# Optimization experiments

Hardware: AMD Instinct MI355X
Metric: run time of the kernel (lower is better)

The kernel has to match this reference:

```python
import jax, jax.numpy as jnp
import numpy as np

N_NODES = 100000
N_EDGES = 600000
HID = 128
N_ETYPES = 8


def setup_inputs() -> dict:
    key = jax.random.key(0)
    ks = jax.random.split(key, 10)
    s = 1.0 / np.sqrt(HID)
    return {
        "h": jax.random.normal(ks[0], (N_NODES, HID), dtype=jnp.float32),
        "edge_index": jax.random.randint(ks[1], (2, N_EDGES), 0, N_NODES, dtype=jnp.int64),
        "edge_type": jax.random.randint(ks[2], (N_EDGES,), 0, N_ETYPES, dtype=jnp.int64),
        # per-edge-type Linear(hidden, hidden): weight (T, H_out, H_in) stored as (T, H_in, H_out) for einsum
        "message_W": jax.random.uniform(ks[3], (N_ETYPES, HID, HID), jnp.float32, -s, s),
        "message_b": jax.random.uniform(ks[4], (N_ETYPES, HID), jnp.float32, -s, s),
        # GRUCell params (torch layout): w_ih (3H, H), w_hh (3H, H), b_ih (3H,), b_hh (3H,)
        "gru_w_ih": jax.random.uniform(ks[5], (3 * HID, HID), jnp.float32, -s, s),
        "gru_w_hh": jax.random.uniform(ks[6], (3 * HID, HID), jnp.float32, -s, s),
        "gru_b_ih": jax.random.uniform(ks[7], (3 * HID,), jnp.float32, -s, s),
        "gru_b_hh": jax.random.uniform(ks[8], (3 * HID,), jnp.float32, -s, s),
    }


def reference(h, edge_index, edge_type, message_W, message_b,
              gru_w_ih, gru_w_hh, gru_b_ih, gru_b_hh):
    num_nodes = h.shape[0]
    src, dst = edge_index[0], edge_index[1]

    # Transform every node by every edge-type Linear once: (N, T, H).
    # Equivalent to per-type msg = h[src] @ W[t].T + b[t] gathered by edge type.
    all_msgs = jnp.einsum('nh,thd->ntd', h, message_W) + message_b  # (N, T, H)
    msg = all_msgs[src, edge_type]                                   # (E, H) gather
    messages = jax.ops.segment_sum(msg, dst, num_segments=num_nodes)  # scatter-add

    # GRUCell: r,z,n gates (torch semantics)
    gi = messages @ gru_w_ih.T + gru_b_ih  # (N, 3H)
    gh = h @ gru_w_hh.T + gru_b_hh         # (N, 3H)
    i_r, i_z, i_n = jnp.split(gi, 3, axis=-1)
    h_r, h_z, h_n = jnp.split(gh, 3, axis=-1)
    r = jax.nn.sigmoid(i_r + h_r)
    z = jax.nn.sigmoid(i_z + h_z)
    n = jnp.tanh(i_n + r * h_n)
    return (1.0 - z) * n + z * h
```

## Files before the change

kernel.cpp:

```cpp
#include <hip/hip_runtime.h>

#define HID 128
#define NTY 8

typedef __attribute__((ext_vector_type(8))) short bf16x8;
typedef __attribute__((ext_vector_type(4))) float f32x4;

__device__ __forceinline__ unsigned short f2bf(float x) {
    unsigned u = __float_as_uint(x);
    u += 0x7FFF + ((u >> 16) & 1);
    return (unsigned short)(u >> 16);
}
__device__ __forceinline__ float bf2f(unsigned short s) {
    return __uint_as_float(((unsigned)s) << 16);
}
__device__ __forceinline__ float sigmoidf_fast(float x) {
    return 1.f / (1.f + __expf(-x));
}
__device__ __forceinline__ float tanhf_fast(float x) {
    return 1.f - 2.f / (1.f + __expf(2.f * x));
}

__global__ void conv_all_kernel(const float* __restrict__ h, unsigned short* __restrict__ hbf, int nh,
                                const float* __restrict__ W, unsigned short* __restrict__ wfr,
                                const float* __restrict__ wih, const float* __restrict__ whh,
                                unsigned short* __restrict__ wpkf,
                                int* __restrict__ sortedT, int capE,
                                int* __restrict__ deg, int N, int* __restrict__ tcnt)
{
    int i = blockIdx.x * 256 + threadIdx.x;
    if (i < nh) { hbf[i] = f2bf(h[i]); return; }
    i -= nh;
    if (i < 131072) {
        int e = i & 7, lane = (i >> 3) & 63, cb = (i >> 9) & 7, kc = (i >> 12) & 3, t = i >> 14;
        int lr = lane & 15, quad = lane >> 4;
        int d = cb * 16 + lr;
        int k = kc * 32 + quad * 8 + e;
        wfr[i] = f2bf(W[(t << 14) + (k << 7) + d]);
        return;
    }
    i -= 131072;
    if (i < 98304) {
        int e = i & 7, lane = (i >> 3) & 63, f = i >> 9;
        int ct = f & 7, fg = f >> 3;
        int g3 = fg % 3, kc = fg / 3;
        int lr = lane & 15, quad = lane >> 4;
        int d = ct * 16 + lr;
        int kk = quad * 8 + e;
        float v;
        if (kc < 4) v = wih[(g3 * 128 + d) * 128 + kc * 32 + kk];
        else        v = whh[(g3 * 128 + d) * 128 + (kc - 4) * 32 + kk];
        wpkf[i] = f2bf(v);
        return;
    }
    i -= 98304;
    if (i < capE) { sortedT[i] = -1; return; }
    i -= capE;
    if (i < N) { deg[i] = 0; return; }
    i -= N;
    if (i < NTY) tcnt[i] = 0;
}

__global__ void hist_kernel(const int* __restrict__ etype, const int* __restrict__ ei,
                            int E, int* __restrict__ tcnt, int* __restrict__ deg) {
    __shared__ int lc[NTY];
    if (threadIdx.x < NTY) lc[threadIdx.x] = 0;
    __syncthreads();
    int stride = gridDim.x * blockDim.x;
    for (int i = blockIdx.x * blockDim.x + threadIdx.x; i < E; i += stride) {
        atomicAdd(&lc[etype[i]], 1);
        if (deg) atomicAdd(&deg[ei[E + i]], 1);
    }
    __syncthreads();
    if (threadIdx.x < NTY) atomicAdd(&tcnt[threadIdx.x], lc[threadIdx.x]);
}

__global__ void scanA_kernel(const int* __restrict__ deg, int* __restrict__ start,
                             int* __restrict__ bsum, int N) {
    __shared__ int s[256];
    int i = blockIdx.x * 256 + threadIdx.x;
    int v = (i < N) ? deg[i] : 0;
    s[threadIdx.x] = v;
    __syncthreads();
    for (int off = 1; off < 256; off <<= 1) {
        int t = (threadIdx.x >= off) ? s[threadIdx.x - off] : 0;
        __syncthreads();
        s[threadIdx.x] += t;
        __syncthreads();
    }
    if (i < N) start[i] = s[threadIdx.x] - v;
    if (threadIdx.x == 255) bsum[blockIdx.x] = s[255];
}

__global__ void scanB_kernel(int* __restrict__ bsum, int nb,
                             const int* __restrict__ tcnt, int* __restrict__ tcur) {
    __shared__ int s[512];
    int tx = threadIdx.x;
    int v = (tx < nb) ? bsum[tx] : 0;
    s[tx] = v;
    __syncthreads();
    for (int off = 1; off < 512; off <<= 1) {
        int t = (tx >= off) ? s[tx - off] : 0;
        __syncthreads();
        s[tx] += t;
        __syncthreads();
    }
    if (tx < nb) bsum[tx] = s[tx] - v;
    if (tx == 0) {
        int off = 0;
        for (int t = 0; t < NTY; ++t) { tcur[t] = off; off += (tcnt[t] + 127) & ~127; }
    }
}

__global__ void scanC_kernel(int* __restrict__ start, const int* __restrict__ bsum,
                             int* __restrict__ dcur, int N, int E) {
    int i = blockIdx.x * 256 + threadIdx.x;
    if (i < N) {
        int v = start[i] + bsum[blockIdx.x];
        start[i] = v;
        dcur[i] = v;
    }
    if (i == 0) start[N] = E;
}

__global__ __launch_bounds__(256) void scatter_agg(
    const int* __restrict__ etype, const int* __restrict__ ei, int E,
    int* __restrict__ tcur, int* __restrict__ dcur,
    int* __restrict__ sortedT, int* __restrict__ q, int mode)
{
    __shared__ int lcnt[NTY];
    __shared__ int lbase[NTY];
    int tx = threadIdx.x;
    int chunk = (E + gridDim.x - 1) / gridDim.x;
    int s = blockIdx.x * chunk;
    int e = s + chunk; if (e > E) e = E;
    if (tx < NTY) lcnt[tx] = 0;
    __syncthreads();
    for (int i = s + tx; i < e; i += 256)
        atomicAdd(&lcnt[etype[i]], 1);
    __syncthreads();
    if (tx < NTY) {
        lbase[tx] = atomicAdd(&tcur[tx], lcnt[tx]);
        lcnt[tx] = 0;
    }
    __syncthreads();
    for (int i = s + tx; i < e; i += 256) {
        int t = etype[i];
        int lp = atomicAdd(&lcnt[t], 1);
        sortedT[lbase[t] + lp] = i;
        if (mode) q[i] = atomicAdd(&dcur[ei[E + i]], 1);
    }
}

__global__ __launch_bounds__(256) void msg_gemm(
    const unsigned short* __restrict__ hbf, const int* __restrict__ ei, int E,
    const int* __restrict__ etype, const unsigned short* __restrict__ wfr,
    const float* __restrict__ bias, const int* __restrict__ sortedT,
    const int* __restrict__ q, unsigned short* __restrict__ M,
    float* __restrict__ msum, int mode)
{
    __shared__ unsigned short hs[128][136];
    __shared__ int srcs[128], aux[128];
    __shared__ int stype;

    int tx = threadIdx.x;
    int base = blockIdx.x * 128;
    if (tx < 128) {
        int id = sortedT[base + tx];
        srcs[tx] = (id >= 0) ? ei[id] : -1;
        aux[tx]  = (id >= 0) ? (mode ? ei[E + id] : q[id]) : -1;
    }
    if (tx == 0) { int id0 = sortedT[base]; stype = (id0 >= 0) ? etype[id0] : -1; }
    __syncthreads();
    int t = stype;
    if (t < 0) return;

    for (int f = tx; f < 2048; f += 256) {
        int row = f >> 4, c8 = (f & 15) * 8;
        int s = srcs[row]; if (s < 0) s = 0;
        *(uint4*)&hs[row][c8] = *(const uint4*)&hbf[(size_t)s * 128 + c8];
    }
    __syncthreads();

    int lane = tx & 63, w = tx >> 6;
    int r0 = (w >> 1) * 64, c0 = (w & 1) * 64;
    int lr = lane & 15, quad = lane >> 4;
    f32x4 acc[4][4] = {};

    const unsigned short* wt = wfr + (t << 14) + ((unsigned)(c0 >> 4) << 9) + (lane << 3);
    #pragma unroll
    for (int kc = 0; kc < 4; ++kc) {
        bf16x8 af[4], wf[4];
        #pragma unroll
        for (int rb = 0; rb < 4; ++rb) af[rb] = *(const bf16x8*)&hs[r0 + rb * 16 + lr][kc * 32 + quad * 8];
        #pragma unroll
        for (int cb = 0; cb < 4; ++cb) wf[cb] = *(const bf16x8*)&wt[(kc << 12) + (cb << 9)];
        #pragma unroll
        for (int rb = 0; rb < 4; ++rb)
            #pragma unroll
            for (int cb = 0; cb < 4; ++cb)
                acc[rb][cb] = __builtin_amdgcn_mfma_f32_16x16x32_bf16(wf[cb], af[rb], acc[rb][cb], 0, 0, 0);
    }

    float4 bv4[4];
    #pragma unroll
    for (int cb = 0; cb < 4; ++cb)
        bv4[cb] = *(const float4*)&bias[t * 128 + c0 + cb * 16 + quad * 4];

    #pragma unroll
    for (int rb = 0; rb < 4; ++rb) {
        int e = r0 + rb * 16 + lr;
        int mr = aux[e];
        if (mr < 0) continue;
        #pragma unroll
        for (int cb = 0; cb < 4; ++cb) {
            int d0 = c0 + cb * 16 + quad * 4;
            f32x4 a = acc[rb][cb];
            if (mode) {
                atomicAdd(&msum[(size_t)mr * 128 + d0 + 0], a[0] + bv4[cb].x);
                atomicAdd(&msum[(size_t)mr * 128 + d0 + 1], a[1] + bv4[cb].y);
                atomicAdd(&msum[(size_t)mr * 128 + d0 + 2], a[2] + bv4[cb].z);
                atomicAdd(&msum[(size_t)mr * 128 + d0 + 3], a[3] + bv4[cb].w);
            } else {
                uint2 v;
                v.x = (unsigned)f2bf(a[0] + bv4[cb].x) | ((unsigned)f2bf(a[1] + bv4[cb].y) << 16);
                v.y = (unsigned)f2bf(a[2] + bv4[cb].z) | ((unsigned)f2bf(a[3] + bv4[cb].w) << 16);
                *(uint2*)&M[(size_t)mr * 128 + d0] = v;
            }
        }
    }
}

__global__ __launch_bounds__(256) void gru_fused(
    const unsigned short* __restrict__ M, const int* __restrict__ start,
    const float* __restrict__ msum_fb, const unsigned short* __restrict__ hbf,
    const unsigned short* __restrict__ wpkf, const float* __restrict__ bih,
    const float* __restrict__ bhh, const float* __restrict__ hf,
    float* __restrict__ out, int N, int mode)
{
    __shared__ unsigned short As[4][2048];

    int tx = threadIdx.x;
    int n0 = blockIdx.x * 64;

    {
        int node = tx >> 2, qd = tx & 3;
        int n = n0 + node;
        int nc = (n < N) ? n : N - 1;
        float a[32];
        #pragma unroll
        for (int j = 0; j < 32; ++j) a[j] = 0.f;
        if (mode == 0) {
            int s = start[nc], e = start[nc + 1];
            uint4 c0v, c1v, c2v, c3v;
            if (s < e) {
                const unsigned short* Mp = M + (size_t)s * 128 + qd * 32;
                c0v = *(const uint4*)(Mp);
                c1v = *(const uint4*)(Mp + 8);
                c2v = *(const uint4*)(Mp + 16);
                c3v = *(const uint4*)(Mp + 24);
            }
            for (int r = s; r < e; ++r) {
                uint4 p0 = c0v, p1 = c1v, p2 = c2v, p3 = c3v;
                if (r + 1 < e) {
                    const unsigned short* Mn = M + (size_t)(r + 1) * 128 + qd * 32;
                    c0v = *(const uint4*)(Mn);
                    c1v = *(const uint4*)(Mn + 8);
                    c2v = *(const uint4*)(Mn + 16);
                    c3v = *(const uint4*)(Mn + 24);
                }
                const unsigned short* q0 = (const unsigned short*)&p0;
                const unsigned short* q1 = (const unsigned short*)&p1;
                const unsigned short* q2 = (const unsigned short*)&p2;
                const unsigned short* q3 = (const unsigned short*)&p3;
                #pragma unroll
                for (int u = 0; u < 8; ++u) {
                    a[u]      += bf2f(q0[u]);
                    a[8 + u]  += bf2f(q1[u]);
                    a[16 + u] += bf2f(q2[u]);
                    a[24 + u] += bf2f(q3[u]);
                }
            }
        } else {
            #pragma unroll
            for (int j = 0; j < 8; ++j) {
                float4 v = *(const float4*)&msum_fb[(size_t)nc * 128 + qd * 32 + j * 4];
                a[j * 4 + 0] = v.x; a[j * 4 + 1] = v.y; a[j * 4 + 2] = v.z; a[j * 4 + 3] = v.w;
            }
        }
        unsigned short tmp[32];
        #pragma unroll
        for (int j = 0; j < 32; ++j) tmp[j] = f2bf(a[j]);
        int lrw = node & 15, wv = node >> 4;
        #pragma unroll
        for (int j = 0; j < 4; ++j) {
            int byte = (lrw << 8) + (qd << 6) + (j << 4);
            byte ^= (lrw & 7) << 4;
            *(uint4*)((char*)&As[wv][0] + byte) = *(const uint4*)&tmp[j * 8];
        }
    }
    __syncthreads();

    int lane = tx & 63, w = tx >> 6;
    int lr = lane & 15, quad = lane >> 4;
    int node = n0 + w * 16 + lr;
    bool valid = node < N;
    int nc = valid ? node : (N - 1);
    unsigned short* AsW = &As[w][0];

    bf16x8 afh[4];
    {
        const unsigned short* hrow = hbf + ((size_t)nc << 7) + (quad << 3);
        #pragma unroll
        for (int k4 = 0; k4 < 4; ++k4) afh[k4] = *(const bf16x8*)&hrow[k4 * 32];
    }
    const unsigned short* wg = wpkf + (lane << 3);

    #pragma unroll
    for (int dh = 0; dh < 2; ++dh) {
        f32x4 aR[4] = {}, aZ[4] = {}, aH[4] = {};
        #pragma unroll
        for (int kc = 0; kc < 8; ++kc) {
            bf16x8 af;
            if (kc < 4) {
                int byte = ((lr << 8) + (kc << 6) + (quad << 4)) ^ ((lr & 7) << 4);
                af = *(const bf16x8*)((char*)AsW + byte);
            } else {
                af = afh[kc - 4];
            }
            #pragma unroll
            for (int c = 0; c < 4; ++c) {
                int ct = dh * 4 + c;
                bf16x8 wfR = *(const bf16x8*)&wg[(unsigned)((kc * 3 + 0) * 8 + ct) << 9];
                aR[c] = __builtin_amdgcn_mfma_f32_16x16x32_bf16(wfR, af, aR[c], 0, 0, 0);
                bf16x8 wfZ = *(const bf16x8*)&wg[(unsigned)((kc * 3 + 1) * 8 + ct) << 9];
                aZ[c] = __builtin_amdgcn_mfma_f32_16x16x32_bf16(wfZ, af, aZ[c], 0, 0, 0);
                if (kc >= 4) {
                    bf16x8 wfH = *(const bf16x8*)&wg[(unsigned)((kc * 3 + 2) * 8 + ct) << 9];
                    aH[c] = __builtin_amdgcn_mfma_f32_16x16x32_bf16(wfH, af, aH[c], 0, 0, 0);
                }
            }
        }
        f32x4 rv[4], zv[4];
        #pragma unroll
        for (int c = 0; c < 4; ++c) {
            int d0 = (dh * 4 + c) * 16 + quad * 4;
            f32x4 bir = *(const f32x4*)&bih[d0],       bhr = *(const f32x4*)&bhh[d0];
            f32x4 biz = *(const f32x4*)&bih[128 + d0], bhz = *(const f32x4*)&bhh[128 + d0];
            f32x4 bin = *(const f32x4*)&bih[256 + d0], bhn = *(const f32x4*)&bhh[256 + d0];
            #pragma unroll
            for (int j = 0; j < 4; ++j) {
                rv[c][j] = sigmoidf_fast(aR[c][j] + bir[j] + bhr[j]);
                zv[c][j] = sigmoidf_fast(aZ[c][j] + biz[j] + bhz[j]);
                aH[c][j] = bin[j] + rv[c][j] * (aH[c][j] + bhn[j]);
            }
        }
        #pragma unroll
        for (int kc = 0; kc < 4; ++kc) {
            int byte = ((lr << 8) + (kc << 6) + (quad << 4)) ^ ((lr & 7) << 4);
            bf16x8 af = *(const bf16x8*)((char*)AsW + byte);
            #pragma unroll
            for (int c = 0; c < 4; ++c) {
                bf16x8 wfH = *(const bf16x8*)&wg[(unsigned)((kc * 3 + 2) * 8 + dh * 4 + c) << 9];
                aH[c] = __builtin_amdgcn_mfma_f32_16x16x32_bf16(wfH, af, aH[c], 0, 0, 0);
            }
        }
        if (valid) {
            #pragma unroll
            for (int c = 0; c < 4; ++c) {
                int d0 = (dh * 4 + c) * 16 + quad * 4;
                f32x4 h0 = *(const f32x4*)&hf[(size_t)node * 128 + d0];
                f32x4 o;
                #pragma unroll
                for (int j = 0; j < 4; ++j) {
                    float nn = tanhf_fast(aH[c][j]);
                    o[j] = (1.f - zv[c][j]) * nn + zv[c][j] * h0[j];
                }
                *(f32x4*)&out[(size_t)node * 128 + d0] = o;
            }
        }
    }
}

extern "C" void kernel_launch(void* const* d_in, const int* in_sizes, int n_in,
                              void* d_out, int out_size, void* d_ws, size_t ws_size,
                              hipStream_t stream)
{
    const float* h     = (const float*)d_in[0];
    const int*   ei    = (const int*)d_in[1];
    const int*   etype = (const int*)d_in[2];
    const float* W     = (const float*)d_in[3];
    const float* b     = (const float*)d_in[4];
    const float* wih   = (const float*)d_in[5];
    const float* whh   = (const float*)d_in[6];
    const float* bih   = (const float*)d_in[7];
    const float* bhh   = (const float*)d_in[8];
    float* out = (float*)d_out;

    int E = in_sizes[1] / 2;
    int N = in_sizes[0] / HID;
    int capE = ((E + 127) / 128 + NTY) * 128;
    int nbA = (N + 255) / 256;

    char* p = (char*)d_ws;
    auto alloc = [&](size_t bytes) { char* r = p; p += (bytes + 255) & ~(size_t)255; return r; };
    unsigned short* hbf  = (unsigned short*)alloc((size_t)N * 128 * 2);
    unsigned short* wfr  = (unsigned short*)alloc((size_t)131072 * 2);
    unsigned short* wpkf = (unsigned short*)alloc((size_t)98304 * 2);
    int* tcnt    = (int*)alloc(NTY * 4);
    int* tcur    = (int*)alloc(NTY * 4);
    int* sortedT = (int*)alloc((size_t)capE * 4);
    unsigned short* M = (unsigned short*)alloc((size_t)E * 128 * 2);
    int* q     = (int*)alloc((size_t)E * 4);
    int* deg   = (int*)alloc((size_t)N * 4);
    int* start = (int*)alloc((size_t)(N + 1) * 4);
    int* dcur  = (int*)alloc((size_t)N * 4);
    int* bsum  = (int*)alloc(512 * 4);
    int mode = ((size_t)(p - (char*)d_ws) <= ws_size) ? 0 : 1;

    if (mode == 1) hipMemsetAsync(out, 0, (size_t)N * 128 * 4, stream);

    int totalConv = N * 128 + 131072 + 98304 + capE + N + NTY;
    conv_all_kernel<<<(totalConv + 255) / 256, 256, 0, stream>>>(
        h, hbf, N * 128, W, wfr, wih, whh, wpkf, sortedT, capE, deg, N, tcnt);

    hist_kernel<<<1024, 256, 0, stream>>>(etype, ei, E, tcnt, (mode == 0) ? deg : nullptr);
    if (mode == 0)
        scanA_kernel<<<nbA, 256, 0, stream>>>(deg, start, bsum, N);
    scanB_kernel<<<1, 512, 0, stream>>>(bsum, nbA, tcnt, tcur);
    if (mode == 0)
        scanC_kernel<<<nbA, 256, 0, stream>>>(start, bsum, dcur, N, E);
    scatter_agg<<<256, 256, 0, stream>>>(etype, ei, E, tcur, dcur, sortedT, q, (mode == 0) ? 1 : 0);

    msg_gemm<<<capE / 128, 256, 0, stream>>>(hbf, ei, E, etype, wfr, b, sortedT, q, M, out, mode);
    gru_fused<<<(N + 63) / 64, 256, 0, stream>>>(M, start, out, hbf, wpkf, bih, bhh, h, out, N, mode);
}
```

Measured before the change: 404.5 us.

## Balance CSR segment reduction across wave lanes with LDS float atomics

Replaces the per-node serial walk over CSR message rows, where four threads each handled a node and the loop length followed that node's degree, with a wave-level sweep. Each wave streams all rows of its 16 nodes in a contiguous range, four rows at a time, and accumulates into an fp32 LDS tile with shared-memory atomics. The GEMM A operand is then converted from fp32 LDS to bf16 with a packed convert instruction. This balances load across lanes when degrees vary, at the cost of many LDS atomics and a larger fp32 LDS footprint that may lower occupancy.

```diff
diff --git a/kernel.cpp b/kernel.cpp
--- a/kernel.cpp
+++ b/kernel.cpp
@@ -19,6 +19,11 @@
 }
 __device__ __forceinline__ float tanhf_fast(float x) {
     return 1.f - 2.f / (1.f + __expf(2.f * x));
+}
+__device__ __forceinline__ unsigned cvt_pk_bf16(float lo, float hi) {
+    unsigned r;
+    asm("v_cvt_pk_bf16_f32 %0, %1, %2" : "=v"(r) : "v"(lo), "v"(hi));
+    return r;
 }
 
 __global__ void conv_all_kernel(const float* __restrict__ h, unsigned short* __restrict__ hbf, int nh,
@@ -238,75 +243,55 @@
     const float* __restrict__ bhh, const float* __restrict__ hf,
     float* __restrict__ out, int N, int mode)
 {
-    __shared__ unsigned short As[4][2048];
+    __shared__ __align__(16) float macc[64][132];
+    __shared__ int bnds_l[65];
 
     int tx = threadIdx.x;
     int n0 = blockIdx.x * 64;
-
-    {
-        int node = tx >> 2, qd = tx & 3;
-        int n = n0 + node;
-        int nc = (n < N) ? n : N - 1;
-        float a[32];
-        #pragma unroll
-        for (int j = 0; j < 32; ++j) a[j] = 0.f;
-        if (mode == 0) {
-            int s = start[nc], e = start[nc + 1];
-            uint4 c0v, c1v, c2v, c3v;
-            if (s < e) {
-                const unsigned short* Mp = M + (size_t)s * 128 + qd * 32;
-                c0v = *(const uint4*)(Mp);
-                c1v = *(const uint4*)(Mp + 8);
-                c2v = *(const uint4*)(Mp + 16);
-                c3v = *(const uint4*)(Mp + 24);
-            }
-            for (int r = s; r < e; ++r) {
-                uint4 p0 = c0v, p1 = c1v, p2 = c2v, p3 = c3v;
-                if (r + 1 < e) {
-                    const unsigned short* Mn = M + (size_t)(r + 1) * 128 + qd * 32;
-                    c0v = *(const uint4*)(Mn);
-                    c1v = *(const uint4*)(Mn + 8);
-                    c2v = *(const uint4*)(Mn + 16);
-                    c3v = *(const uint4*)(Mn + 24);
-                }
-                const unsigned short* q0 = (const unsigned short*)&p0;
-                const unsigned short* q1 = (const unsigned short*)&p1;
-                const unsigned short* q2 = (const unsigned short*)&p2;
-                const unsigned short* q3 = (const unsigned short*)&p3;
-                #pragma unroll
-                for (int u = 0; u < 8; ++u) {
-                    a[u]      += bf2f(q0[u]);
-                    a[8 + u]  += bf2f(q1[u]);
-                    a[16 + u] += bf2f(q2[u]);
-                    a[24 + u] += bf2f(q3[u]);
-                }
-            }
-        } else {
-            #pragma unroll
-            for (int j = 0; j < 8; ++j) {
-                float4 v = *(const float4*)&msum_fb[(size_t)nc * 128 + qd * 32 + j * 4];
-                a[j * 4 + 0] = v.x; a[j * 4 + 1] = v.y; a[j * 4 + 2] = v.z; a[j * 4 + 3] = v.w;
-            }
-        }
-        unsigned short tmp[32];
-        #pragma unroll
-        for (int j = 0; j < 32; ++j) tmp[j] = f2bf(a[j]);
-        int lrw = node & 15, wv = node >> 4;
-        #pragma unroll
-        for (int j = 0; j < 4; ++j) {
-            int byte = (lrw << 8) + (qd << 6) + (j << 4);
-            byte ^= (lrw & 7) << 4;
-            *(uint4*)((char*)&As[wv][0] + byte) = *(const uint4*)&tmp[j * 8];
-        }
-    }
-    __syncthreads();
-
     int lane = tx & 63, w = tx >> 6;
     int lr = lane & 15, quad = lane >> 4;
+
+    for (int i = tx; i < 64 * 132 / 4; i += 256)
+        ((f32x4*)macc)[i] = f32x4{0.f, 0.f, 0.f, 0.f};
+    if (mode == 0 && tx <= 64) {
+        int idx = n0 + tx; if (idx > N) idx = N;
+        bnds_l[tx] = start[idx];
+    }
+    __syncthreads();
+
+    if (mode == 0) {
+        int row_off = quad;
+        int c = lr;
+        int lo = bnds_l[w * 16], hi = bnds_l[w * 16 + 16];
+        int cur = w * 16;
+        int nxt = bnds_l[cur + 1];
+        int r = lo + row_off;
+        uint4 v = {};
+        if (r < hi) v = *(const uint4*)&M[(size_t)r * 128 + c * 8];
+        while (r < hi) {
+            int rn = r + 4;
+            uint4 vn = {};
+            if (rn < hi) vn = *(const uint4*)&M[(size_t)rn * 128 + c * 8];
+            while (r >= nxt) { ++cur; nxt = bnds_l[cur + 1]; }
+            const unsigned short* pv = (const unsigned short*)&v;
+            float* mrow = &macc[cur][c * 8];
+            #pragma unroll
+            for (int j = 0; j < 8; ++j) atomicAdd(&mrow[j], bf2f(pv[j]));
+            v = vn; r = rn;
+        }
+    } else {
+        for (int i = tx; i < 2048; i += 256) {
+            int node = i >> 5, q4 = (i & 31) * 4;
+            int n = n0 + node; int nc2 = (n < N) ? n : N - 1;
+            *(f32x4*)&macc[node][q4] = *(const f32x4*)&msum_fb[(size_t)nc2 * 128 + q4];
+        }
+    }
+    __syncthreads();
+
     int node = n0 + w * 16 + lr;
+    int mrow_i = w * 16 + lr;
     bool valid = node < N;
     int nc = valid ? node : (N - 1);
-    unsigned short* AsW = &As[w][0];
 
     bf16x8 afh[4];
     {
@@ -323,58 +308,70 @@
         for (int kc = 0; kc < 8; ++kc) {
             bf16x8 af;
             if (kc < 4) {
-                int byte = ((lr << 8) + (kc << 6) + (quad << 4)) ^ ((lr & 7) << 4);
-                af = *(const bf16x8*)((char*)AsW + byte);
+                const float* mp = &macc[mrow_i][kc * 32 + quad * 8];
+                f32x4 L = *(const f32x4*)mp, H = *(const f32x4*)(mp + 4);
+                int4 au;
+                au.x = (int)cvt_pk_bf16(L[0], L[1]);
+                au.y = (int)cvt_pk_bf16(L[2], L[3]);
+                au.z = (int)cvt_pk_bf16(H[0], H[1]);
+                au.w = (int)cvt_pk_bf16(H[2], H[3]);
+                af = *(const bf16x8*)&au;
             } else {
                 af = afh[kc - 4];
             }
             #pragma unroll
-            for (int c = 0; c < 4; ++c) {
-                int ct = dh * 4 + c;
+            for (int cg = 0; cg < 4; ++cg) {
+                int ct = dh * 4 + cg;
                 bf16x8 wfR = *(const bf16x8*)&wg[(unsigned)((kc * 3 + 0) * 8 + ct) << 9];
-                aR[c] = __builtin_amdgcn_mfma_f32_16x16x32_bf16(wfR, af, aR[c], 0, 0, 0);
+                aR[cg] = __builtin_amdgcn_mfma_f32_16x16x32_bf16(wfR, af, aR[cg], 0, 0, 0);
                 bf16x8 wfZ = *(const bf16x8*)&wg[(unsigned)((kc * 3 + 1) * 8 + ct) << 9];
-                aZ[c] = __builtin_amdgcn_mfma_f32_16x16x32_bf16(wfZ, af, aZ[c], 0, 0, 0);
+                aZ[cg] = __builtin_amdgcn_mfma_f32_16x16x32_bf16(wfZ, af, aZ[cg], 0, 0, 0);
                 if (kc >= 4) {
                     bf16x8 wfH = *(const bf16x8*)&wg[(unsigned)((kc * 3 + 2) * 8 + ct) << 9];
-                    aH[c] = __builtin_amdgcn_mfma_f32_16x16x32_bf16(wfH, af, aH[c], 0, 0, 0);
+                    aH[cg] = __builtin_amdgcn_mfma_f32_16x16x32_bf16(wfH, af, aH[cg], 0, 0, 0);
                 }
             }
         }
         f32x4 rv[4], zv[4];
         #pragma unroll
-        for (int c = 0; c < 4; ++c) {
-            int d0 = (dh * 4 + c) * 16 + quad * 4;
+        for (int cg = 0; cg < 4; ++cg) {
+            int d0 = (dh * 4 + cg) * 16 + quad * 4;
             f32x4 bir = *(const f32x4*)&bih[d0],       bhr = *(const f32x4*)&bhh[d0];
             f32x4 biz = *(const f32x4*)&bih[128 + d0], bhz = *(const f32x4*)&bhh[128 + d0];
             f32x4 bin = *(const f32x4*)&bih[256 + d0], bhn = *(const f32x4*)&bhh[256 + d0];
             #pragma unroll
             for (int j = 0; j < 4; ++j) {
-                rv[c][j] = sigmoidf_fast(aR[c][j] + bir[j] + bhr[j]);
-                zv[c][j] = sigmoidf_fast(aZ[c][j] + biz[j] + bhz[j]);
-                aH[c][j] = bin[j] + rv[c][j] * (aH[c][j] + bhn[j]);
+                rv[cg][j] = sigmoidf_fast(aR[cg][j] + bir[j] + bhr[j]);
+                zv[cg][j] = sigmoidf_fast(aZ[cg][j] + biz[j] + bhz[j]);
+                aH[cg][j] = bin[j] + rv[cg][j] * (aH[cg][j] + bhn[j]);
             }
         }
         #pragma unroll
         for (int kc = 0; kc < 4; ++kc) {
-            int byte = ((lr << 8) + (kc << 6) + (quad << 4)) ^ ((lr & 7) << 4);
-            bf16x8 af = *(const bf16x8*)((char*)AsW + byte);
-            #pragma unroll
-            for (int c = 0; c < 4; ++c) {
-                bf16x8 wfH = *(const bf16x8*)&wg[(unsigned)((kc * 3 + 2) * 8 + dh * 4 + c) << 9];
-                aH[c] = __builtin_amdgcn_mfma_f32_16x16x32_bf16(wfH, af, aH[c], 0, 0, 0);
+            const float* mp = &macc[mrow_i][kc * 32 + quad * 8];
+            f32x4 L = *(const f32x4*)mp, H = *(const f32x4*)(mp + 4);
+            int4 au;
+            au.x = (int)cvt_pk_bf16(L[0], L[1]);
+            au.y = (int)cvt_pk_bf16(L[2], L[3]);
+            au.z = (int)cvt_pk_bf16(H[0], H[1]);
+            au.w = (int)cvt_pk_bf16(H[2], H[3]);
+            bf16x8 af = *(const bf16x8*)&au;
+            #pragma unroll
+            for (int cg = 0; cg < 4; ++cg) {
+                bf16x8 wfH = *(const bf16x8*)&wg[(unsigned)((kc * 3 + 2) * 8 + dh * 4 + cg) << 9];
+                aH[cg] = __builtin_amdgcn_mfma_f32_16x16x32_bf16(wfH, af, aH[cg], 0, 0, 0);
             }
         }
         if (valid) {
             #pragma unroll
-            for (int c = 0; c < 4; ++c) {
-                int d0 = (dh * 4 + c) * 16 + quad * 4;
+            for (int cg = 0; cg < 4; ++cg) {
+                int d0 = (dh * 4 + cg) * 16 + quad * 4;
                 f32x4 h0 = *(const f32x4*)&hf[(size_t)node * 128 + d0];
                 f32x4 o;
                 #pragma unroll
                 for (int j = 0; j < 4; ++j) {
-                    float nn = tanhf_fast(aH[c][j]);
-                    o[j] = (1.f - zv[c][j]) * nn + zv[c][j] * h0[j];
+                    float nn = tanhf_fast(aH[cg][j]);
+                    o[j] = (1.f - zv[cg][j]) * nn + zv[cg][j] * h0[j];
                 }
                 *(f32x4*)&out[(size_t)node * 128 + d0] = o;
             }
```

After: 735.8 us. 81.9% more time.

## Stage dst-sorted message rows cooperatively in LDS before per-node reduction

Applied to the files above, without the earlier changes.

Instead of each node's four threads walking their own CSR segment of the message buffer with per-thread software prefetch, the block now loads its contiguous 64-node row range in 128-row chunks into shared memory using coalesced loads from all threads. Each thread then sums its slice from LDS. This is meant to turn irregular, latency-bound per-thread global reads into coalesced block loads. In exchange it adds about 35 KB of LDS, which may lower occupancy, and extra block-wide barriers per chunk.

```diff
diff --git a/kernel.cpp b/kernel.cpp
--- a/kernel.cpp
+++ b/kernel.cpp
@@ -238,60 +238,66 @@
     const float* __restrict__ bhh, const float* __restrict__ hf,
     float* __restrict__ out, int N, int mode)
 {
+    __shared__ unsigned short chunkb[128][136];
     __shared__ unsigned short As[4][2048];
+    __shared__ int bnds_l[65];
 
     int tx = threadIdx.x;
     int n0 = blockIdx.x * 64;
 
+    if (tx <= 64) {
+        int idx = n0 + tx; if (idx > N) idx = N;
+        bnds_l[tx] = (mode == 0) ? start[idx] : 0;
+    }
+    __syncthreads();
+
+    int ln = tx >> 2, qd = tx & 3;
+    float a[32];
+    #pragma unroll
+    for (int j = 0; j < 32; ++j) a[j] = 0.f;
+
+    if (mode == 0) {
+        int rowlo = bnds_l[0], rowhi = bnds_l[64];
+        int sn = bnds_l[ln], en = bnds_l[ln + 1];
+        for (int cbase = rowlo; cbase < rowhi; cbase += 128) {
+            int cend = cbase + 128; if (cend > rowhi) cend = rowhi;
+            #pragma unroll
+            for (int it = 0; it < 8; ++it) {
+                int i = tx + it * 256;
+                int row = cbase + (i >> 4);
+                if (row < cend)
+                    *(uint4*)&chunkb[i >> 4][(i & 15) * 8] =
+                        *(const uint4*)&M[(size_t)row * 128 + (i & 15) * 8];
+            }
+            __syncthreads();
+            int lo = sn > cbase ? sn : cbase;
+            int hi = en < cend ? en : cend;
+            for (int r = lo; r < hi; ++r) {
+                const unsigned short* mp = &chunkb[r - cbase][qd * 32];
+                #pragma unroll
+                for (int u = 0; u < 4; ++u) {
+                    uint4 v = *(const uint4*)&mp[u * 8];
+                    const unsigned short* pv = (const unsigned short*)&v;
+                    #pragma unroll
+                    for (int j = 0; j < 8; ++j) a[u * 8 + j] += bf2f(pv[j]);
+                }
+            }
+            __syncthreads();
+        }
+    } else {
+        int n = n0 + ln; int nc2 = (n < N) ? n : N - 1;
+        #pragma unroll
+        for (int j = 0; j < 8; ++j) {
+            float4 v = *(const float4*)&msum_fb[(size_t)nc2 * 128 + qd * 32 + j * 4];
+            a[j * 4 + 0] = v.x; a[j * 4 + 1] = v.y; a[j * 4 + 2] = v.z; a[j * 4 + 3] = v.w;
+        }
+    }
+
     {
-        int node = tx >> 2, qd = tx & 3;
-        int n = n0 + node;
-        int nc = (n < N) ? n : N - 1;
-        float a[32];
-        #pragma unroll
-        for (int j = 0; j < 32; ++j) a[j] = 0.f;
-        if (mode == 0) {
-            int s = start[nc], e = start[nc + 1];
-            uint4 c0v, c1v, c2v, c3v;
-            if (s < e) {
-                const unsigned short* Mp = M + (size_t)s * 128 + qd * 32;
-                c0v = *(const uint4*)(Mp);
-                c1v = *(const uint4*)(Mp + 8);
-                c2v = *(const uint4*)(Mp + 16);
-                c3v = *(const uint4*)(Mp + 24);
-            }
-            for (int r = s; r < e; ++r) {
-                uint4 p0 = c0v, p1 = c1v, p2 = c2v, p3 = c3v;
-                if (r + 1 < e) {
-                    const unsigned short* Mn = M + (size_t)(r + 1) * 128 + qd * 32;
-                    c0v = *(const uint4*)(Mn);
-                    c1v = *(const uint4*)(Mn + 8);
-                    c2v = *(const uint4*)(Mn + 16);
-                    c3v = *(const uint4*)(Mn + 24);
-                }
-                const unsigned short* q0 = (const unsigned short*)&p0;
-                const unsigned short* q1 = (const unsigned short*)&p1;
-                const unsigned short* q2 = (const unsigned short*)&p2;
-                const unsigned short* q3 = (const unsigned short*)&p3;
-                #pragma unroll
-                for (int u = 0; u < 8; ++u) {
-                    a[u]      += bf2f(q0[u]);
-                    a[8 + u]  += bf2f(q1[u]);
-                    a[16 + u] += bf2f(q2[u]);
-                    a[24 + u] += bf2f(q3[u]);
-                }
-            }
-        } else {
-            #pragma unroll
-            for (int j = 0; j < 8; ++j) {
-                float4 v = *(const float4*)&msum_fb[(size_t)nc * 128 + qd * 32 + j * 4];
-                a[j * 4 + 0] = v.x; a[j * 4 + 1] = v.y; a[j * 4 + 2] = v.z; a[j * 4 + 3] = v.w;
-            }
-        }
         unsigned short tmp[32];
         #pragma unroll
         for (int j = 0; j < 32; ++j) tmp[j] = f2bf(a[j]);
-        int lrw = node & 15, wv = node >> 4;
+        int lrw = ln & 15, wv = ln >> 4;
         #pragma unroll
         for (int j = 0; j < 4; ++j) {
             int byte = (lrw << 8) + (qd << 6) + (j << 4);
```

After: 456.5 us. 1.13x slower.
